# Kernel tuning notes

Measured on AMD Instinct MI355X. Metric: run time of the kernel, lower is better.

The kernel has to match this reference:

```python
import jax, jax.numpy as jnp
import numpy as np

B, T, C = 4, 1024, 2048
H, N = 32, 64
D_DECAY, D_AAA, D_MV, D_GATE = 96, 96, 64, 256


def setup_inputs() -> dict:
    key = jax.random.key(0)
    ks = iter(jax.random.split(key, 48))

    def rn(shape, s):
        return jax.random.normal(next(ks), shape, jnp.float32) * s

    inp = {
        "x": rn((B, T, C), 1.0),
        "shift_state_in": rn((B, C), 1.0),
        "wkv_state_in": jnp.zeros((B, H, N, N), jnp.float32),
        "v_first_val": rn((B, T, C), 1.0),
    }
    for nme in ["x_r", "x_w", "x_k", "x_v", "x_a", "x_g"]:
        inp[nme] = rn((C,), 0.2) + 0.5
    inp["w0"] = rn((C,), 0.3) - 4.0  # log-log decay bias, keeps decay in (0,1)
    inp["w1"] = rn((C, D_DECAY), 0.02)
    inp["w2"] = rn((D_DECAY, C), 0.02)
    inp["a0"] = rn((C,), 0.1)
    inp["a1"] = rn((C, D_AAA), 0.02)
    inp["a2"] = rn((D_AAA, C), 0.02)
    inp["v0"] = jnp.ones((C,), jnp.float32)
    inp["v1"] = rn((C, D_MV), 0.02)
    inp["v2"] = rn((D_MV, C), 0.02)
    inp["g1"] = rn((C, D_GATE), 0.02)
    inp["g2"] = rn((D_GATE, C), 0.02)
    inp["k_k"] = jnp.full((C,), 0.85, jnp.float32)
    inp["k_a"] = jnp.ones((C,), jnp.float32)
    inp["r_k"] = rn((H, N), 0.02)
    s = 1.0 / float(np.sqrt(C))
    for nme in ["Wr", "Wk", "Wv", "Wo"]:
        inp[nme] = rn((C, C), s)
    inp["ln_w"] = jnp.ones((C,), jnp.float32)
    inp["ln_b"] = jnp.zeros((C,), jnp.float32)
    return inp


def _forward(x, shift_state_in, wkv_state_in, v_first_val,
             x_r, x_w, x_k, x_v, x_a, x_g,
             w0, w1, w2, a0, a1, a2, v0, v1, v2, g1, g2,
             k_k, k_a, r_k, Wr, Wk, Wv, Wo, ln_w, ln_b):
    Bs, Ts, Cs = x.shape
    shift_state_out = x[:, -1]
    # token shift
    xprev = jnp.concatenate([shift_state_in[:, None, :], x[:, :-1]], axis=1)
    dx = xprev - x
    xr = x + dx * x_r
    xw = x + dx * x_w
    xk = x + dx * x_k
    xv = x + dx * x_v
    xa = x + dx * x_a
    xg = x + dx * x_g
    r = xr @ Wr.T
    k = xk @ Wk.T
    v = xv @ Wv.T
    # soft-clamped log-log decay: w in (-inf, -0.5], decay = exp(-exp(w)) in (0,1)
    w_log = -jax.nn.softplus(-(w0 + jnp.tanh(xw @ w1) @ w2)) - 0.5
    decay = jnp.exp(-jnp.exp(w_log))
    a = jax.nn.sigmoid(a0 + (xa @ a1) @ a2)  # in-context learning rate
    g = jax.nn.sigmoid(xg @ g1) @ g2          # output gate
    # removal key: per-head L2-normalized
    kk = (k * k_k).reshape(Bs, Ts, H, N)
    kk = kk / jnp.maximum(jnp.linalg.norm(kk, axis=-1, keepdims=True), 1e-12)
    kk = kk.reshape(Bs, Ts, Cs)
    k = k * (1.0 + (a - 1.0) * k_a)
    # layer_id > 0: value residual mixing with first-layer values
    v = v + (v_first_val - v) * jax.nn.sigmoid(v0 + (xv @ v1) @ v2)
    v_first_out = v_first_val

    # [B,T,C] -> [T,B,H,N] for scan
    def th(t):
        return t.reshape(Bs, Ts, H, N).transpose(1, 0, 2, 3)

    r_s, w_s, k_s, v_s, kk_s, a_s = map(th, (r, decay, k, v, kk, a))

    def step(state, inp):
        rt, wt, kt, vt, kkt, at = inp  # each [B,H,N]
        # state: [B,H,N_value,N_key]
        sab = jnp.einsum('bhvn,bhn,bhm->bhvm', state, -kkt, kkt * at)
        state = state * wt[:, :, None, :] + sab + vt[..., None] * kt[:, :, None, :]
        yt = jnp.einsum('bhvn,bhn->bhv', state, rt)
        return state, yt

    wkv_state_out, y = jax.lax.scan(step, wkv_state_in, (r_s, w_s, k_s, v_s, kk_s, a_s))
    y = y.transpose(1, 0, 2, 3)  # [B,T,H,N]

    # GroupNorm over each head (eps = 1e-5 * head_size)
    eps = 1e-5 * N
    mu = y.mean(-1, keepdims=True)
    var = y.var(-1, keepdims=True)
    yn = (y - mu) / jnp.sqrt(var + eps)
    yn = yn * ln_w.reshape(H, N) + ln_b.reshape(H, N)
    yn = yn.reshape(Bs, Ts, Cs)

    rr = r.reshape(Bs, Ts, H, N)
    kh = k.reshape(Bs, Ts, H, N)
    vh = v.reshape(Bs, Ts, H, N)
    bonus = ((rr * kh * r_k).sum(-1, keepdims=True) * vh).reshape(Bs, Ts, Cs)
    out = ((yn + bonus) * g) @ Wo.T
    return out, shift_state_out, wkv_state_out, v_first_out


def reference(x, shift_state_in, wkv_state_in, v_first_val,
              x_r, x_w, x_k, x_v, x_a, x_g,
              w0, w1, w2, a0, a1, a2, v0, v1, v2, g1, g2,
              k_k, k_a, r_k, Wr, Wk, Wv, Wo, ln_w, ln_b):
    return _forward(x, shift_state_in, wkv_state_in, v_first_val,
                    x_r, x_w, x_k, x_v, x_a, x_g,
                    w0, w1, w2, a0, a1, a2, v0, v1, v2, g1, g2,
                    k_k, k_a, r_k, Wr, Wk, Wv, Wo, ln_w, ln_b)
```

## Files before the change

### kernel.cpp

```cpp
#include <hip/hip_runtime.h>
#include <hip/hip_bf16.h>
#include <stdint.h>

typedef unsigned short u16;
typedef unsigned int u32;
typedef unsigned long long u64;
typedef __attribute__((ext_vector_type(8))) short short8;
typedef __attribute__((ext_vector_type(4))) float f32x4;
typedef __attribute__((ext_vector_type(2))) unsigned int u32x2;

#define BB 4
#define TT 1024
#define CC 2048

__device__ __forceinline__ u16 f2bf(float f){
  __hip_bfloat16 h = __float2bfloat16(f);
  return *reinterpret_cast<u16*>(&h);
}
__device__ __forceinline__ float bf2f(u16 h){
  union { u32 u; float f; } v; v.u = ((u32)h) << 16; return v.f;
}
__device__ __forceinline__ float bflo(u32 p){
  union { u32 u; float f; } v; v.u = p << 16; return v.f;
}
__device__ __forceinline__ float bfhi(u32 p){
  union { u32 u; float f; } v; v.u = p & 0xFFFF0000u; return v.f;
}

__device__ __forceinline__ void gload16(const void* g, void* s){
  __builtin_amdgcn_global_load_lds((const __attribute__((address_space(1))) u32*)g,
                                   (__attribute__((address_space(3))) u32*)s, 16, 0, 0);
}

__device__ __forceinline__ float wave_sum64(float x){
  #pragma unroll
  for (int m = 1; m < 64; m <<= 1) x += __shfl_xor(x, m, 64);
  return x;
}

template<int N>
__device__ __forceinline__ float ror_add(float x){
  int t = __builtin_amdgcn_update_dpp(0, __builtin_bit_cast(int, x), 0x120 | N, 0xF, 0xF, false);
  return x + __builtin_bit_cast(float, t);
}
__device__ __forceinline__ float red16(float x){
  x = ror_add<8>(x); x = ror_add<4>(x); x = ror_add<2>(x); x = ror_add<1>(x);
  return x;
}

__device__ __forceinline__ void xcd_map(int nx, int& bx, int& row0){
  const int G = gridDim.x;
  const int q = G >> 3, r = G & 7;
  const int xcd = blockIdx.x & 7, i2 = blockIdx.x >> 3;
  const int sw = (xcd < r) ? (xcd*(q+1) + i2) : (r*(q+1) + (xcd - r)*q + i2);
  const int by = sw / nx;
  bx = sw - by*nx;
  row0 = by * 128;
}

__global__ __launch_bounds__(256) void k_wprep(
  const float* __restrict__ wr, const float* __restrict__ wk,
  const float* __restrict__ wv, const float* __restrict__ wo,
  const float* __restrict__ w1, const float* __restrict__ a1,
  const float* __restrict__ v1, const float* __restrict__ g1,
  const float* __restrict__ w2, const float* __restrict__ a2,
  const float* __restrict__ v2, const float* __restrict__ g2,
  u16* __restrict__ wsb)
{
  __shared__ float lds[32][33];
  const int blk0 = blockIdx.x;
  if (blk0 < 16384){
    int i = blk0*256 + threadIdx.x;
    int seg = i >> 20;
    int off = (i & 1048575) * 4;
    const float* src = (seg==0) ? wr : (seg==1) ? wk : (seg==2) ? wv : wo;
    const size_t dofs = (seg==0) ? 4194304u : (seg==1) ? 8388608u : (seg==2) ? 12582912u : 0u;
    float4 v = *(const float4*)&src[off];
    *(ushort4*)&wsb[dofs + off] = make_ushort4(f2bf(v.x), f2bf(v.y), f2bf(v.z), f2bf(v.w));
    return;
  }
  const int blk = blk0 - 16384;
  const float* src; int R, S, Rpad, tile, tiles_r; size_t dst;
  if      (blk <  256){ src=w1; R=2048; S=96;   Rpad=2048; dst=16777216u; tile=blk;      tiles_r=64; }
  else if (blk <  512){ src=a1; R=2048; S=96;   Rpad=2048; dst=17039360u; tile=blk-256;  tiles_r=64; }
  else if (blk <  768){ src=v1; R=2048; S=64;   Rpad=2048; dst=17301504u; tile=blk-512;  tiles_r=64; }
  else if (blk < 1280){ src=g1; R=2048; S=256;  Rpad=2048; dst=17563648u; tile=blk-768;  tiles_r=64; }
  else if (blk < 1536){ src=w2; R=96;   S=2048; Rpad=128;  dst=18087936u; tile=blk-1280; tiles_r=4;  }
  else if (blk < 1792){ src=a2; R=96;   S=2048; Rpad=128;  dst=18350080u; tile=blk-1536; tiles_r=4;  }
  else if (blk < 2048){ src=v2; R=64;   S=2048; Rpad=128;  dst=18612224u; tile=blk-1792; tiles_r=4;  }
  else                { src=g2; R=256;  S=2048; Rpad=256;  dst=18874368u; tile=blk-2048; tiles_r=8;  }
  const int tr = tile % tiles_r, ts = tile / tiles_r;
  const int r0 = tr*32, s0 = ts*32;
  const int tj = threadIdx.x & 31, ti = threadIdx.x >> 5;
  #pragma unroll
  for (int p=0;p<4;p++){
    int rr = r0 + p*8 + ti, ss = s0 + tj;
    lds[p*8+ti][tj] = (rr < R && ss < S) ? src[(size_t)rr*S + ss] : 0.f;
  }
  __syncthreads();
  #pragma unroll
  for (int p=0;p<4;p++){
    int sl = p*8 + ti, rl = tj;
    wsb[dst + (size_t)(s0+sl)*Rpad + r0 + rl] = f2bf(lds[rl][sl]);
  }
}

__global__ __launch_bounds__(256) void k_prep4(
  const float* __restrict__ x, const float* __restrict__ shift_in,
  const float* __restrict__ mr, const float* __restrict__ mk,
  const float* __restrict__ mv, const float* __restrict__ mw,
  u16* __restrict__ xr, u16* __restrict__ xk, u16* __restrict__ xv, u16* __restrict__ xw)
{
  int idx = blockIdx.x*256 + threadIdx.x;
  int c4 = (idx & 511) * 4;
  int t  = (idx >> 9) & (TT-1);
  int b  = idx >> 19;
  size_t xo = ((size_t)(b*TT + t))*CC + c4;
  float4 xc = *(const float4*)&x[xo];
  float4 xp = (t == 0) ? *(const float4*)&shift_in[(size_t)b*CC + c4]
                       : *(const float4*)&x[xo - CC];
  float d0 = xp.x-xc.x, d1 = xp.y-xc.y, d2 = xp.z-xc.z, d3 = xp.w-xc.w;
#define MIXO(mp, op) { float4 m = *(const float4*)&mp[c4]; \
    *(ushort4*)&op[xo] = make_ushort4(f2bf(fmaf(d0,m.x,xc.x)), f2bf(fmaf(d1,m.y,xc.y)), \
                                      f2bf(fmaf(d2,m.z,xc.z)), f2bf(fmaf(d3,m.w,xc.w))); }
  MIXO(mr, xr); MIXO(mk, xk); MIXO(mv, xv); MIXO(mw, xw);
#undef MIXO
}

template<int AMODE>
__device__ __forceinline__ void gemm_body(
  const u16* __restrict__ Abf,
  const float* __restrict__ xg, const float* __restrict__ shiftg,
  const float* __restrict__ ma, const float* __restrict__ mg,
  const u16* __restrict__ Bt, float* __restrict__ Cf, u16* __restrict__ Cb,
  int K, int lda, int ldb, int ldc, int nx)
{
  __shared__ alignas(16) u16 sA[128*64];
  __shared__ alignas(16) u16 sB[128*64];
  const int tid = threadIdx.x;
  const int wv = tid >> 6, ln = tid & 63;
  int bx, row0;
  xcd_map(nx, bx, row0);
  const int wr = wv >> 1, wc = wv & 1;

  const float* mixv = nullptr;
  const u16* Ap = Abf;
  const u16* Btp = Bt;
  u16* Cbp = Cb;
  bool bmix = false;
  int bcol0 = bx * 128;
  int ccol0 = bx * 128;
  int ldaa = lda, ldbb = ldb, ldcc = ldc;
  int KK = K, act = 0;

  if (AMODE == 2){
    if (bx < 48){
      int sel = bx >> 4;
      Ap = Abf + (size_t)sel * 8388608u;
      Cbp = Cb + (size_t)sel * 8388608u;
      ccol0 = (bx & 15) * 128;
      ldcc = 2048; ldaa = 2048;
    } else {
      int sb = bx - 48;
      Cbp = (u16*)Cf;
      ccol0 = sb * 128;
      ldcc = 640;
      act = (sb==0) ? 1 : (sb>=3 ? 2 : 0);
      if (sb == 0){ Ap = Abf + 25165824u; ldaa = 2048; }
      else if (sb == 2){ Ap = Abf + 16777216u; ldaa = 2048; }
      else { bmix = true; mixv = (sb==1) ? ma : mg; }
    }
  }
  if (AMODE == 3){
    int sel = bx >> 4;
    Ap = Abf + sel*128;
    Btp = Bt + (size_t)sel * 262144u;
    ldbb = (sel==3) ? 256 : 128;
    KK = (sel==3) ? 256 : 128;
    const int coffs[4] = {0, 8388608, 17842176, 26230784};
    Cbp = Cb + coffs[sel];
    ccol0 = (bx & 15) * 128;
    bcol0 = ccol0;
    ldcc = 2048;
  }

  f32x4 acc[4][4] = {};
  const int srow = ln >> 3;
  const int scol = ((ln & 7) ^ srow) * 8;
  const int ob0  = wv * 4096;
  const int rsw  = (ln & 7) << 3;

  for (int k0 = 0; k0 < KK; k0 += 64){
    __syncthreads();
    if (AMODE != 2 || !bmix){
      #pragma unroll
      for (int j=0;j<4;j++)
        gload16(&Ap[(size_t)(row0 + wv*32 + j*8 + srow)*ldaa + k0 + scol],
                (void*)((char*)sA + ob0 + j*1024));
    }
    #pragma unroll
    for (int j=0;j<4;j++)
      gload16(&Btp[(size_t)(bcol0 + wv*32 + j*8 + srow)*ldbb + k0 + scol],
              (void*)((char*)sB + ob0 + j*1024));
    if (AMODE == 2 && bmix){
      const int r_  = tid >> 2;
      const int akc = (tid & 3) * 8;
      #pragma unroll
      for (int kb2 = 0; kb2 < 64; kb2 += 32){
        float4 m0 = *(const float4*)&mixv[k0 + kb2 + akc];
        float4 m1 = *(const float4*)&mixv[k0 + kb2 + akc + 4];
        #pragma unroll
        for (int it = 0; it < 2; ++it){
          int r = r_ + it*64;
          int gr = row0 + r;
          size_t xo = (size_t)gr*CC + k0 + kb2 + akc;
          float4 c0 = *(const float4*)&xg[xo];
          float4 c1 = *(const float4*)&xg[xo + 4];
          const float* pp = ((gr & (TT-1)) == 0) ? &shiftg[(size_t)(gr >> 10)*CC + k0 + kb2 + akc]
                                                 : &xg[xo - CC];
          float4 p0 = *(const float4*)&pp[0];
          float4 p1 = *(const float4*)&pp[4];
          short8 vvv;
          vvv[0] = (short)f2bf(c0.x + (p0.x - c0.x)*m0.x);
          vvv[1] = (short)f2bf(c0.y + (p0.y - c0.y)*m0.y);
          vvv[2] = (short)f2bf(c0.z + (p0.z - c0.z)*m0.z);
          vvv[3] = (short)f2bf(c0.w + (p0.w - c0.w)*m0.w);
          vvv[4] = (short)f2bf(c1.x + (p1.x - c1.x)*m1.x);
          vvv[5] = (short)f2bf(c1.y + (p1.y - c1.y)*m1.y);
          vvv[6] = (short)f2bf(c1.z + (p1.z - c1.z)*m1.z);
          vvv[7] = (short)f2bf(c1.w + (p1.w - c1.w)*m1.w);
          int csw = (kb2 + akc) ^ ((r & 7) << 3);
          *(short8*)&sA[r*64 + csw] = vvv;
        }
      }
    }
    __syncthreads();
    #pragma unroll
    for (int kk = 0; kk < 2; ++kk){
      short8 aF[4], bF[4];
      #pragma unroll
      for (int m=0;m<4;m++){
        int rr = wr*64 + m*16 + (ln&15);
        aF[m] = *(const short8*)&sA[rr*64 + ((kk*32 + (ln>>4)*8) ^ rsw)];
      }
      #pragma unroll
      for (int n=0;n<4;n++){
        int rr = wc*64 + n*16 + (ln&15);
        bF[n] = *(const short8*)&sB[rr*64 + ((kk*32 + (ln>>4)*8) ^ rsw)];
      }
      #pragma unroll
      for (int m=0;m<4;m++)
        #pragma unroll
        for (int n=0;n<4;n++)
          acc[m][n] = __builtin_amdgcn_mfma_f32_16x16x32_bf16(aF[m], bF[n], acc[m][n], 0,0,0);
    }
  }

  const int cr = (ln >> 4) * 4, ccol = ln & 15;
  #pragma unroll
  for (int m=0;m<4;m++){
    #pragma unroll
    for (int n=0;n<4;n++){
      int gc = ccol0 + wc*64 + n*16 + ccol;
      #pragma unroll
      for (int j=0;j<4;j++){
        int gr = row0 + wr*64 + m*16 + cr + j;
        float v = acc[m][n][j];
        if (AMODE == 0){
          Cf[(size_t)gr*ldcc + gc] = v;
        } else {
          if (act == 1) v = tanhf(v);
          else if (act == 2) v = 1.f/(1.f + expf(-v));
          Cbp[(size_t)gr*ldcc + gc] = f2bf(v);
        }
      }
    }
  }
}

__global__ __launch_bounds__(256) void k_gemm_rkv(
  const u16* Abf, const float* xg, const float* shiftg, const float* ma, const float* mg,
  const u16* Bt, float* Cf, u16* Cb, int K, int lda, int ldb, int ldc, int nx)
{ gemm_body<2>(Abf, xg, shiftg, ma, mg, Bt, Cf, Cb, K, lda, ldb, ldc, nx); }

__global__ __launch_bounds__(256) void k_gemm_s2(
  const u16* Abf, const float* xg, const float* shiftg, const float* ma, const float* mg,
  const u16* Bt, float* Cf, u16* Cb, int K, int lda, int ldb, int ldc, int nx)
{ gemm_body<3>(Abf, xg, shiftg, ma, mg, Bt, Cf, Cb, K, lda, ldb, ldc, nx); }

__global__ __launch_bounds__(256) void k_gemm_fin(
  const u16* Abf, const float* xg, const float* shiftg, const float* ma, const float* mg,
  const u16* Bt, float* Cf, u16* Cb, int K, int lda, int ldb, int ldc, int nx)
{ gemm_body<0>(Abf, xg, shiftg, ma, mg, Bt, Cf, Cb, K, lda, ldb, ldc, nx); }

__global__ __launch_bounds__(256) void k_post1(
  u16* __restrict__ kb, u16* __restrict__ vb, const u16* __restrict__ winb,
  u16* __restrict__ ainb, u16* __restrict__ vinb,
  const float* __restrict__ vfirst,
  const float* __restrict__ w0, const float* __restrict__ a0, const float* __restrict__ v0,
  const float* __restrict__ kkv, const float* __restrict__ kav,
  float* __restrict__ dec)
{
  int grp = blockIdx.x*4 + (threadIdx.x >> 6);
  int n = threadIdx.x & 63;
  int i = grp >> 5, h = grp & 31;
  int c = h*64 + n;
  size_t idx = (size_t)i*CC + c;
  float k  = bf2f(kb[idx]),  v = bf2f(vb[idx]);
  float wi = bf2f(winb[idx]), ai = bf2f(ainb[idx]), vi = bf2f(vinb[idx]);
  float vf = vfirst[idx];
  float a  = 1.f/(1.f + expf(-(a0[c] + ai)));
  float z  = -(w0[c] + wi);
  float sp = (z > 15.f) ? z : log1pf(expf(z));
  float decay = expf(-expf(-sp - 0.5f));
  float vg = 1.f/(1.f + expf(-(v0[c] + vi)));
  float vfin = v + (vf - v)*vg;
  float kkr = k * kkv[c];
  float ss = wave_sum64(kkr*kkr);
  float kkn = kkr / fmaxf(sqrtf(ss), 1e-12f);
  float kfin = k * (1.f + (a - 1.f)*kav[c]);
  kb[idx] = f2bf(kfin);
  vb[idx] = f2bf(vfin);
  dec[idx] = decay;
  vinb[idx] = f2bf(kkn);
  ainb[idx] = f2bf(-(kkn * a));
}

#define SDECL(S) float4 w##S[8]; u32x2 b##S[8], k##S[8], kk##S[8], r##S[8]; u32 v##S[8];

#define SISSUE(S, t0) do {                                                        \
  _Pragma("unroll")                                                               \
  for (int s_=0; s_<8; ++s_){                                                     \
    u64 ow = (u64)(uintptr_t)&wb [gc0 + (size_t)((t0)+s_)*CC];                    \
    u64 ob = (u64)(uintptr_t)&bbp[gc0 + (size_t)((t0)+s_)*CC];                    \
    u64 ok = (u64)(uintptr_t)&kb [gc0 + (size_t)((t0)+s_)*CC];                    \
    u64 oq = (u64)(uintptr_t)&kkb[gc0 + (size_t)((t0)+s_)*CC];                    \
    u64 orr= (u64)(uintptr_t)&rb [gc0 + (size_t)((t0)+s_)*CC];                    \
    u64 ov = (u64)(uintptr_t)&vb [gv0 + (size_t)((t0)+s_)*CC];                    \
    asm volatile("global_load_dwordx4 %0, %1, off" : "=v"(w##S[s_])  : "v"(ow) : "memory"); \
    asm volatile("global_load_dwordx2 %0, %1, off" : "=v"(b##S[s_])  : "v"(ob) : "memory"); \
    asm volatile("global_load_dwordx2 %0, %1, off" : "=v"(k##S[s_])  : "v"(ok) : "memory"); \
    asm volatile("global_load_dwordx2 %0, %1, off" : "=v"(kk##S[s_]) : "v"(oq) : "memory"); \
    asm volatile("global_load_dwordx2 %0, %1, off" : "=v"(r##S[s_])  : "v"(orr): "memory"); \
    asm volatile("global_load_dword   %0, %1, off" : "=v"(v##S[s_])  : "v"(ov) : "memory"); \
  }                                                                               \
} while(0)

#define SCHUNK(S, t0, CNT) do {                                                   \
  asm volatile("s_waitcnt vmcnt(" #CNT ")" ::: "memory");                         \
  __builtin_amdgcn_sched_barrier(0);                                              \
  _Pragma("unroll")                                                               \
  for (int s_=0; s_<8; ++s_){                                                     \
    const float w_0=w##S[s_].x, w_1=w##S[s_].y, w_2=w##S[s_].z, w_3=w##S[s_].w;   \
    const float b_0=bflo(b##S[s_].x), b_1=bfhi(b##S[s_].x),                       \
                b_2=bflo(b##S[s_].y), b_3=bfhi(b##S[s_].y);                       \
    const float k_0=bflo(k##S[s_].x), k_1=bfhi(k##S[s_].x),                       \
                k_2=bflo(k##S[s_].y), k_3=bfhi(k##S[s_].y);                       \
    const float q_0=bflo(kk##S[s_].x), q_1=bfhi(kk##S[s_].x),                     \
                q_2=bflo(kk##S[s_].y), q_3=bfhi(kk##S[s_].y);                     \
    const float r_0=bflo(r##S[s_].x), r_1=bfhi(r##S[s_].x),                       \
                r_2=bflo(r##S[s_].y), r_3=bfhi(r##S[s_].y);                       \
    const float vv0_ = bflo(v##S[s_]);                                            \
    const float vv1_ = bfhi(v##S[s_]);                                            \
    float p0_ = fmaf(st[0][0],q_0, st[0][1]*q_1) + fmaf(st[0][2],q_2, st[0][3]*q_3); \
    float p1_ = fmaf(st[1][0],q_0, st[1][1]*q_1) + fmaf(st[1][2],q_2, st[1][3]*q_3); \
    p0_ = red16(p0_); p1_ = red16(p1_);                                           \
    st[0][0] = fmaf(st[0][0],w_0, fmaf(p0_,b_0, vv0_*k_0));                       \
    st[0][1] = fmaf(st[0][1],w_1, fmaf(p0_,b_1, vv0_*k_1));                       \
    st[0][2] = fmaf(st[0][2],w_2, fmaf(p0_,b_2, vv0_*k_2));                       \
    st[0][3] = fmaf(st[0][3],w_3, fmaf(p0_,b_3, vv0_*k_3));                       \
    st[1][0] = fmaf(st[1][0],w_0, fmaf(p1_,b_0, vv1_*k_0));                       \
    st[1][1] = fmaf(st[1][1],w_1, fmaf(p1_,b_1, vv1_*k_1));                       \
    st[1][2] = fmaf(st[1][2],w_2, fmaf(p1_,b_2, vv1_*k_2));                       \
    st[1][3] = fmaf(st[1][3],w_3, fmaf(p1_,b_3, vv1_*k_3));                       \
    float y0_ = fmaf(st[0][0],r_0, st[0][1]*r_1) + fmaf(st[0][2],r_2, st[0][3]*r_3); \
    float y1_ = fmaf(st[1][0],r_0, st[1][1]*r_1) + fmaf(st[1][2],r_2, st[1][3]*r_3); \
    y0_ = red16(y0_); y1_ = red16(y1_);                                           \
    if (cg == 0){                                                                 \
      u32 pk_ = (u32)f2bf(y0_) | ((u32)f2bf(y1_) << 16);                          \
      *(u32*)&yb[gv0 + (size_t)((t0)+s_)*CC] = pk_;                               \
    }                                                                             \
  }                                                                               \
} while(0)

__global__ __launch_bounds__(64, 1) void k_scan(
  const u16* __restrict__ rb, const float* __restrict__ wb,
  const u16* __restrict__ kb, const u16* __restrict__ vb,
  const u16* __restrict__ kkb, const u16* __restrict__ bbp,
  const float* __restrict__ wkv_in, u16* __restrict__ yb, float* __restrict__ wkv_out)
{
  const int blk = blockIdx.x;
  const int bh = blk & 127, oct = blk >> 7;
  const int b = bh >> 5, h = bh & 31;
  const int ln = threadIdx.x;
  const int rg = ln >> 4;
  const int cg = ln & 15;
  const int row0 = oct*8 + rg*2;
  const int col0 = cg*4;

  float st[2][4];
  {
    const float* sp0 = &wkv_in[((size_t)bh*64 + row0    )*64 + col0];
    const float* sp1 = &wkv_in[((size_t)bh*64 + row0 + 1)*64 + col0];
    float4 a = *(const float4*)sp0, c = *(const float4*)sp1;
    st[0][0]=a.x; st[0][1]=a.y; st[0][2]=a.z; st[0][3]=a.w;
    st[1][0]=c.x; st[1][1]=c.y; st[1][2]=c.z; st[1][3]=c.w;
  }

  const size_t gc0 = ((size_t)b*TT)*CC + h*64 + col0;
  const size_t gv0 = ((size_t)b*TT)*CC + h*64 + row0;

  SDECL(A) SDECL(B)

  SISSUE(A, 0);
  SISSUE(B, 8);
  SCHUNK(A, 0, 48);
  SISSUE(A, 16);
  SCHUNK(B, 8, 56);
  SISSUE(B, 24);
  for (int c = 1; c < 63; ++c){
    const int t0 = c*16;
    SCHUNK(A, t0, 56);
    SISSUE(A, t0+16);
    SCHUNK(B, t0+8, 56);
    SISSUE(B, t0+24);
  }
  SCHUNK(A, 1008, 56);
  SCHUNK(B, 1016, 0);

  {
    float* wo0 = &wkv_out[((size_t)bh*64 + row0    )*64 + col0];
    float* wo1 = &wkv_out[((size_t)bh*64 + row0 + 1)*64 + col0];
    *(float4*)wo0 = make_float4(st[0][0], st[0][1], st[0][2], st[0][3]);
    *(float4*)wo1 = make_float4(st[1][0], st[1][1], st[1][2], st[1][3]);
  }
}

__global__ __launch_bounds__(256) void k_post2(
  const u16* __restrict__ ybuf, const u16* __restrict__ rbuf,
  const u16* __restrict__ kfb, const u16* __restrict__ vfb,
  const u16* __restrict__ gbuf, const float* __restrict__ rk,
  const float* __restrict__ lnw, const float* __restrict__ lnb, u16* __restrict__ ao)
{
  int grp = blockIdx.x*4 + (threadIdx.x >> 6);
  int n = threadIdx.x & 63;
  int i = grp >> 5, h = grp & 31;
  int c = h*64 + n;
  size_t idx = (size_t)i*CC + c;
  float y = bf2f(ybuf[idx]);
  float s1 = wave_sum64(y);
  float s2 = wave_sum64(y*y);
  float mu = s1 * (1.f/64.f);
  float var = s2 * (1.f/64.f) - mu*mu;
  float yn = (y - mu) * rsqrtf(var + 6.4e-4f) * lnw[c] + lnb[c];
  float rv = bf2f(rbuf[idx]), kv = bf2f(kfb[idx]);
  float s3 = wave_sum64(rv * kv * rk[c]);
  float bonus = s3 * bf2f(vfb[idx]);
  ao[idx] = f2bf((yn + bonus) * bf2f(gbuf[idx]));
}

__global__ __launch_bounds__(256) void k_shift(const float* __restrict__ x, float* __restrict__ so){
  int i = blockIdx.x*256 + threadIdx.x;
  int b = i >> 9, c4 = (i & 511)*4;
  *(float4*)&so[(size_t)b*CC + c4] = *(const float4*)&x[((size_t)(b*TT + TT-1))*CC + c4];
}

extern "C" void kernel_launch(void* const* d_in, const int* in_sizes, int n_in,
                              void* d_out, int out_size, void* d_ws, size_t ws_size,
                              hipStream_t stream)
{
  const float* x        = (const float*)d_in[0];
  const float* shift_in = (const float*)d_in[1];
  const float* wkv_in   = (const float*)d_in[2];
  const float* v_first  = (const float*)d_in[3];
  const float* x_r = (const float*)d_in[4];
  const float* x_w = (const float*)d_in[5];
  const float* x_k = (const float*)d_in[6];
  const float* x_v = (const float*)d_in[7];
  const float* x_a = (const float*)d_in[8];
  const float* x_g = (const float*)d_in[9];
  const float* w0 = (const float*)d_in[10];
  const float* w1 = (const float*)d_in[11];
  const float* w2 = (const float*)d_in[12];
  const float* a0 = (const float*)d_in[13];
  const float* a1 = (const float*)d_in[14];
  const float* a2 = (const float*)d_in[15];
  const float* v0 = (const float*)d_in[16];
  const float* v1 = (const float*)d_in[17];
  const float* v2 = (const float*)d_in[18];
  const float* g1 = (const float*)d_in[19];
  const float* g2 = (const float*)d_in[20];
  const float* k_k = (const float*)d_in[21];
  const float* k_a = (const float*)d_in[22];
  const float* r_k = (const float*)d_in[23];
  const float* Wr = (const float*)d_in[24];
  const float* Wk = (const float*)d_in[25];
  const float* Wv = (const float*)d_in[26];
  const float* Wo = (const float*)d_in[27];
  const float* ln_w = (const float*)d_in[28];
  const float* ln_b = (const float*)d_in[29];

  char* ws = (char*)d_ws;
  u16* WOB  = (u16*)(ws + 0);
  u16* WRB  = (u16*)(ws + 8388608);
  u16* B2W  = (u16*)(ws + 36175872);
  u16* PBUF = (u16*)(ws + 38797312);
  u16* RB   = (u16*)(ws + 44040192);
  u16* KB   = (u16*)(ws + 60817408);
  u16* VB   = (u16*)(ws + 77594624);
  u16* YB   = (u16*)(ws + 94371840);
  float* DEC  = (float*)(ws + 8388608);
  u16* AO   = (u16*)(ws + 8388608);

  float* out       = (float*)d_out;
  float* shift_out = out + 8388608;
  float* wkv_out   = out + 8396800;
  float* vf_out    = out + 8921088;
  u16* XRKV = (u16*)d_out;
  u16* WINb = (u16*)d_out;
  u16* AINb = (u16*)((char*)d_out + 16777216);
  u16* VINb = (u16*)((char*)d_out + 35684352);

  k_wprep<<<18944, 256, 0, stream>>>(Wr, Wk, Wv, Wo, w1, a1, v1, g1, w2, a2, v2, g2, (u16*)ws);

  k_prep4<<<8192, 256, 0, stream>>>(x, shift_in, x_r, x_k, x_v, x_w,
                                    XRKV, XRKV + 8388608u, XRKV + 16777216u, XRKV + 25165824u);

  k_gemm_rkv<<<1696, 256, 0, stream>>>(XRKV, x, shift_in, x_a, x_g,
                                       WRB, (float*)PBUF, RB, 2048, 2048, 2048, 2048, 53);

  k_gemm_s2<<<2048, 256, 0, stream>>>(PBUF, nullptr, nullptr, nullptr, nullptr,
                                      B2W, nullptr, (u16*)d_out, 0, 640, 128, 2048, 64);

  k_post1<<<32768, 256, 0, stream>>>(KB, VB, WINb, AINb, VINb, v_first,
                                     w0, a0, v0, k_k, k_a, DEC);

  k_scan<<<1024, 64, 0, stream>>>(RB, DEC, KB, VB, VINb, AINb, wkv_in, YB, wkv_out);

  k_post2<<<32768, 256, 0, stream>>>(YB, RB, KB, VB, (u16*)((char*)d_out + 52461568),
                                     r_k, ln_w, ln_b, AO);

  k_gemm_fin<<<512, 256, 0, stream>>>(AO, nullptr, nullptr, nullptr, nullptr,
                                      WOB, out, nullptr, 2048, 2048, 2048, 2048, 16);

  k_shift<<<8, 256, 0, stream>>>(x, shift_out);
  hipMemcpyAsync(vf_out, v_first, 33554432, hipMemcpyDeviceToDevice, stream);
}
```

Baseline: 666.5 us.

## Double-buffer LDS tiles in GEMM body to overlap global loads with MFMA

The non-mixing GEMM paths now use two LDS buffers per operand. The next K-tile is prefetched with direct-to-LDS loads, and explicit vmcnt waits let that load overlap the MFMA compute on the current tile. The fused token-mix path keeps the original single-buffered loop. This doubles LDS use per block, which may lower occupancy, and it relies on the hand-written waitcnt counts being correct.

New measurement: 664.3 us, median of 2. No clear change (-0.3%).

```diff
diff --git a/kernel.cpp b/kernel.cpp
--- a/kernel.cpp
+++ b/kernel.cpp
@@ -135,8 +135,8 @@
   const u16* __restrict__ Bt, float* __restrict__ Cf, u16* __restrict__ Cb,
   int K, int lda, int ldb, int ldc, int nx)
 {
-  __shared__ alignas(16) u16 sA[128*64];
-  __shared__ alignas(16) u16 sB[128*64];
+  __shared__ alignas(16) u16 sA[2*128*64];
+  __shared__ alignas(16) u16 sB[2*128*64];
   const int tid = threadIdx.x;
   const int wv = tid >> 6, ln = tid & 63;
   int bx, row0;
@@ -190,19 +190,60 @@
   const int ob0  = wv * 4096;
   const int rsw  = (ln & 7) << 3;
 
-  for (int k0 = 0; k0 < KK; k0 += 64){
-    __syncthreads();
-    if (AMODE != 2 || !bmix){
+  if (AMODE != 2 || !bmix){
+    const int NT = KK >> 6;
+    auto STAGE = [&](int q, int k0){
       #pragma unroll
       for (int j=0;j<4;j++)
         gload16(&Ap[(size_t)(row0 + wv*32 + j*8 + srow)*ldaa + k0 + scol],
-                (void*)((char*)sA + ob0 + j*1024));
+                (void*)((char*)sA + q*16384 + ob0 + j*1024));
+      #pragma unroll
+      for (int j=0;j<4;j++)
+        gload16(&Btp[(size_t)(bcol0 + wv*32 + j*8 + srow)*ldbb + k0 + scol],
+                (void*)((char*)sB + q*16384 + ob0 + j*1024));
+    };
+    STAGE(0, 0);
+    for (int t = 0; t < NT; ++t){
+      const int cur = t & 1;
+      if (t+1 < NT){
+        STAGE(cur^1, (t+1) << 6);
+        asm volatile("s_waitcnt vmcnt(8)" ::: "memory");
+      } else {
+        asm volatile("s_waitcnt vmcnt(0)" ::: "memory");
+      }
+      __builtin_amdgcn_s_barrier();
+      __builtin_amdgcn_sched_barrier(0);
+      const u16* sAq = sA + cur*8192;
+      const u16* sBq = sB + cur*8192;
+      #pragma unroll
+      for (int kk = 0; kk < 2; ++kk){
+        short8 aF[4], bF[4];
+        #pragma unroll
+        for (int m=0;m<4;m++){
+          int rr = wr*64 + m*16 + (ln&15);
+          aF[m] = *(const short8*)&sAq[rr*64 + ((kk*32 + (ln>>4)*8) ^ rsw)];
+        }
+        #pragma unroll
+        for (int n=0;n<4;n++){
+          int rr = wc*64 + n*16 + (ln&15);
+          bF[n] = *(const short8*)&sBq[rr*64 + ((kk*32 + (ln>>4)*8) ^ rsw)];
+        }
+        #pragma unroll
+        for (int m=0;m<4;m++)
+          #pragma unroll
+          for (int n=0;n<4;n++)
+            acc[m][n] = __builtin_amdgcn_mfma_f32_16x16x32_bf16(aF[m], bF[n], acc[m][n], 0,0,0);
+      }
+      __builtin_amdgcn_s_barrier();
+      __builtin_amdgcn_sched_barrier(0);
     }
-    #pragma unroll
-    for (int j=0;j<4;j++)
-      gload16(&Btp[(size_t)(bcol0 + wv*32 + j*8 + srow)*ldbb + k0 + scol],
-              (void*)((char*)sB + ob0 + j*1024));
-    if (AMODE == 2 && bmix){
+  } else {
+    for (int k0 = 0; k0 < KK; k0 += 64){
+      __syncthreads();
+      #pragma unroll
+      for (int j=0;j<4;j++)
+        gload16(&Btp[(size_t)(bcol0 + wv*32 + j*8 + srow)*ldbb + k0 + scol],
+                (void*)((char*)sB + ob0 + j*1024));
       const int r_  = tid >> 2;
       const int akc = (tid & 3) * 8;
       #pragma unroll
@@ -233,26 +274,26 @@
           *(short8*)&sA[r*64 + csw] = vvv;
         }
       }
-    }
-    __syncthreads();
-    #pragma unroll
-    for (int kk = 0; kk < 2; ++kk){
-      short8 aF[4], bF[4];
-      #pragma unroll
-      for (int m=0;m<4;m++){
-        int rr = wr*64 + m*16 + (ln&15);
-        aF[m] = *(const short8*)&sA[rr*64 + ((kk*32 + (ln>>4)*8) ^ rsw)];
+      __syncthreads();
+      #pragma unroll
+      for (int kk = 0; kk < 2; ++kk){
+        short8 aF[4], bF[4];
+        #pragma unroll
+        for (int m=0;m<4;m++){
+          int rr = wr*64 + m*16 + (ln&15);
+          aF[m] = *(const short8*)&sA[rr*64 + ((kk*32 + (ln>>4)*8) ^ rsw)];
+        }
+        #pragma unroll
+        for (int n=0;n<4;n++){
+          int rr = wc*64 + n*16 + (ln&15);
+          bF[n] = *(const short8*)&sB[rr*64 + ((kk*32 + (ln>>4)*8) ^ rsw)];
+        }
+        #pragma unroll
+        for (int m=0;m<4;m++)
+          #pragma unroll
+          for (int n=0;n<4;n++)
+            acc[m][n] = __builtin_amdgcn_mfma_f32_16x16x32_bf16(aF[m], bF[n], acc[m][n], 0,0,0);
       }
-      #pragma unroll
-      for (int n=0;n<4;n++){
-        int rr = wc*64 + n*16 + (ln&15);
-        bF[n] = *(const short8*)&sB[rr*64 + ((kk*32 + (ln>>4)*8) ^ rsw)];
-      }
-      #pragma unroll
-      for (int m=0;m<4;m++)
-        #pragma unroll
-        for (int n=0;n<4;n++)
-          acc[m][n] = __builtin_amdgcn_mfma_f32_16x16x32_bf16(aF[m], bF[n], acc[m][n], 0,0,0);
     }
   }
 
```
